# Performance work log

Measured on AMD Instinct MI355X. Metric: run time of the kernel, lower is better.

The kernel has to match this reference:

```python
import jax, jax.numpy as jnp
import numpy as np

E = 128        # EMBEDDING_DIM
H = 8          # HEAD_NUM
K = 16         # KEY_DIM
NODE = 200     # NODE_SIZE
CLIP = 10.0    # LOGIT_CLIPPING
B = 256
G = 200        # group size
S = 100        # solution tokens


def setup_inputs() -> dict:
    key = jax.random.key(0)
    ks = jax.random.split(key, 9)
    sc = 1.0 / np.sqrt(E)
    return {
        "graph": jax.random.normal(ks[0], (B, 1, E), jnp.float32),
        "capacity": jax.random.uniform(ks[1], (B, G), jnp.float32),
        "sols_mask_pomo": jnp.zeros((B, G, S), jnp.float32),
        "ninf_mask": jnp.zeros((B, G, NODE), jnp.float32),
        "encoded_nodes": jax.random.normal(ks[2], (B, NODE + S, E), jnp.float32),
        "Wq": jax.random.normal(ks[3], (1 + E, H * K), jnp.float32) * sc,
        "Wk": jax.random.normal(ks[4], (E, H * K), jnp.float32) * sc,
        "Wv": jax.random.normal(ks[5], (E, H * K), jnp.float32) * sc,
        "Wc": jax.random.normal(ks[6], (H * K, E), jnp.float32) * sc,
        "bc": jax.random.normal(ks[7], (E,), jnp.float32) * sc,
        "Wk_logit": jax.random.normal(ks[8], (E, E), jnp.float32) * sc,
    }


def _heads(x):
    # [B, C, H*K] -> [B, H, C, K]
    b, c, _ = x.shape
    return x.reshape(b, c, H, K).transpose(0, 2, 1, 3)


def _mha(q, k, v, group_ninf_mask):
    # q: [B,H,n,K], k/v: [B,H,m,K], mask: [B,n,m]
    score = jnp.einsum("bhnk,bhmk->bhnm", q, k) / np.sqrt(K)
    score = score + group_ninf_mask[:, None, :, :]
    w = jax.nn.softmax(score, axis=-1)
    out = jnp.einsum("bhnm,bhmk->bhnk", w, v)          # [B,H,n,K]
    b, _, n, _ = out.shape
    return out.transpose(0, 2, 1, 3).reshape(b, n, H * K)


def reference(graph, capacity, sols_mask_pomo, ninf_mask, encoded_nodes,
              Wq, Wk, Wv, Wc, bc, Wk_logit):
    nodes, sols = encoded_nodes[:, :NODE], encoded_nodes[:, NODE:]
    # reset(): NOTE original uses Wk/Wv for solution tokens too
    k = _heads(nodes @ Wk)
    v = _heads(nodes @ Wv)
    k_s = _heads(sols @ Wk)
    v_s = _heads(sols @ Wv)
    single_head_key = nodes @ Wk_logit                   # [B, NODE, E]

    b, g = capacity.shape
    inp = jnp.concatenate(
        [jnp.broadcast_to(graph, (b, g, E)), capacity[:, :, None]], axis=2)
    q = _heads(inp @ Wq)                                 # [B,H,G,K]

    out_n = _mha(q, k, v, ninf_mask)
    out_s = _mha(q, k_s, v_s, sols_mask_pomo)
    mh = (out_n + out_s) @ Wc + bc                       # [B,G,E]

    score = jnp.einsum("bge,bne->bgn", mh, single_head_key) / np.sqrt(E)
    score = CLIP * jnp.tanh(score) + ninf_mask
    return jax.nn.softmax(score, axis=2)
```

## Files before the change

kernel.cpp:

```cpp
#include <hip/hip_runtime.h>

#define B_    256
#define G_    200
#define S_    100
#define NODE_ 200
#define E_    128
#define H_    8
#define M_    300
#define MT_   19
#define NT_   13

typedef float    f32x4 __attribute__((ext_vector_type(4)));
typedef short    s16x4 __attribute__((ext_vector_type(4)));
typedef short    s16x8 __attribute__((ext_vector_type(8)));
typedef unsigned u32x4 __attribute__((ext_vector_type(4)));

#define MFMA16(A, B, C) __builtin_amdgcn_mfma_f32_16x16x32_bf16(A, B, C, 0, 0, 0)

#define LOG2E_  1.4426950408889634f
#define CQ_     0.36067376022224085f
#define C2T_    0.25503901628148863f
#define C10L_   14.426950408889634f

__device__ __forceinline__ unsigned bf16u(float x) {
    unsigned u = __builtin_bit_cast(unsigned, x);
    return (u + 0x7fffu + ((u >> 16) & 1u)) >> 16;
}
__device__ __forceinline__ float bfbits(unsigned hb16) {
    return __builtin_bit_cast(float, hb16 << 16);
}
__device__ __forceinline__ short bfhi(float x) { return (short)bf16u(x); }
__device__ __forceinline__ short bflo(float x, short hi) {
    float hf = __builtin_bit_cast(float, ((unsigned)(unsigned short)hi) << 16);
    return (short)bf16u(x - hf);
}
__device__ __forceinline__ unsigned cvtpk(float a, float b) {
    unsigned r;
    asm("v_cvt_pk_bf16_f32 %0, %1, %2" : "=v"(r) : "v"(a), "v"(b));
    return r;
}
__device__ __forceinline__ float exp2a(float x) {
    float r;
    asm("v_exp_f32 %0, %1" : "=v"(r) : "v"(x));
    return r;
}
__device__ __forceinline__ s16x8 cat8(s16x4 a, s16x4 b) {
    s16x8 r; r[0]=a[0]; r[1]=a[1]; r[2]=a[2]; r[3]=a[3];
             r[4]=b[0]; r[5]=b[1]; r[6]=b[2]; r[7]=b[3]; return r;
}
__device__ __forceinline__ void split_pack(f32x4 v, s16x8& B1, s16x8& B2) {
    unsigned h01 = cvtpk(v[0], v[1]);
    unsigned h23 = cvtpk(v[2], v[3]);
    float e0 = v[0] - __builtin_bit_cast(float, h01 << 16);
    float e1 = v[1] - __builtin_bit_cast(float, h01 & 0xffff0000u);
    float e2 = v[2] - __builtin_bit_cast(float, h23 << 16);
    float e3 = v[3] - __builtin_bit_cast(float, h23 & 0xffff0000u);
    unsigned l01 = cvtpk(e0, e1), l23 = cvtpk(e2, e3);
    u32x4 w1 = {h01, h23, l01, l23};
    u32x4 w2 = {l01, l23, h01, h23};
    B1 = __builtin_bit_cast(s16x8, w1);
    B2 = __builtin_bit_cast(s16x8, w2);
}
__device__ __forceinline__ void pack8(f32x4 a0, f32x4 a1, s16x8& Bh, s16x8& Bl) {
    unsigned ha = cvtpk(a0[0], a0[1]), hb = cvtpk(a0[2], a0[3]);
    unsigned hc = cvtpk(a1[0], a1[1]), hd = cvtpk(a1[2], a1[3]);
    float e0 = a0[0] - __builtin_bit_cast(float, ha << 16);
    float e1 = a0[1] - __builtin_bit_cast(float, ha & 0xffff0000u);
    float e2 = a0[2] - __builtin_bit_cast(float, hb << 16);
    float e3 = a0[3] - __builtin_bit_cast(float, hb & 0xffff0000u);
    float e4 = a1[0] - __builtin_bit_cast(float, hc << 16);
    float e5 = a1[1] - __builtin_bit_cast(float, hc & 0xffff0000u);
    float e6 = a1[2] - __builtin_bit_cast(float, hd << 16);
    float e7 = a1[3] - __builtin_bit_cast(float, hd & 0xffff0000u);
    unsigned la = cvtpk(e0, e1), lb = cvtpk(e2, e3);
    unsigned lc = cvtpk(e4, e5), ld = cvtpk(e6, e7);
    u32x4 wh = {ha, hb, hc, hd}, wl = {la, lb, lc, ld};
    Bh = __builtin_bit_cast(s16x8, wh);
    Bl = __builtin_bit_cast(s16x8, wl);
}

__global__ __launch_bounds__(64) void wfrag_kernel(
    const float* __restrict__ Wk, const float* __restrict__ Wv,
    const float* __restrict__ Wl, const float* __restrict__ Wc,
    short* __restrict__ wf8_hi, short* __restrict__ wf8_lo)
{
    const int p = blockIdx.x, ct = blockIdx.y;
    const int l = threadIdx.x, qq = l >> 4, li = l & 15;
    const float* W = (p == 0) ? Wk : ((p == 1) ? Wv : ((p == 2) ? Wl : Wc));
    for (int kc = 0; kc < 8; ++kc) {
        s16x4 hi, lo;
        #pragma unroll
        for (int j = 0; j < 4; ++j) {
            float v = W[(kc*16 + qq*4 + j)*E_ + ct*16 + li];
            short h = bfhi(v); hi[j] = h; lo[j] = bflo(v, h);
        }
        const int ix = (((p*8 + ct)*4 + (kc >> 1))*64 + l)*8 + (kc & 1)*4;
        *(s16x4*)(wf8_hi + ix) = hi;
        *(s16x4*)(wf8_lo + ix) = lo;
    }
}

__global__ __launch_bounds__(128) void qbase_kernel(
    const float* __restrict__ graph, const float* __restrict__ Wq,
    float* __restrict__ qbase)
{
    const int b = blockIdx.x, c = threadIdx.x;
    __shared__ float gs[E_];
    gs[c] = graph[b*E_ + c];
    __syncthreads();
    float acc = 0.f;
    #pragma unroll 8
    for (int e = 0; e < E_; ++e) acc += gs[e] * Wq[e*E_ + c];
    qbase[b*E_ + c] = acc;
}

__global__ __launch_bounds__(64, 4) void proj_kernel(
    const float* __restrict__ enc,
    const short* __restrict__ wf8_hi, const short* __restrict__ wf8_lo,
    short* __restrict__ kf_il, short* __restrict__ vf_il,
    short* __restrict__ sf8_hi, short* __restrict__ sf8_lo)
{
    int id = blockIdx.x;
    { const int xcd = id & 7, pos = id >> 3; id = xcd*608 + pos; }
    const int b = id / MT_, mt = id % MT_;
    const int l = threadIdx.x, qq = l >> 4, li = l & 15;
    const int m = mt*16 + li;

    s16x8 Ahi[4], Alo[4];
    #pragma unroll
    for (int u = 0; u < 4; ++u) {
        float va[8];
        if (m < M_) {
            const float* ep = enc + ((size_t)b*M_ + m)*E_ + u*32 + qq*4;
            float4 f0 = *(const float4*)ep;
            float4 f1 = *(const float4*)(ep + 16);
            va[0]=f0.x; va[1]=f0.y; va[2]=f0.z; va[3]=f0.w;
            va[4]=f1.x; va[5]=f1.y; va[6]=f1.z; va[7]=f1.w;
        } else {
            #pragma unroll
            for (int j = 0; j < 8; ++j) va[j] = 0.f;
        }
        #pragma unroll
        for (int j = 0; j < 8; ++j) {
            short h = bfhi(va[j]); Ahi[u][j] = h; Alo[u][j] = bflo(va[j], h);
        }
    }

    __shared__ unsigned tile[16*17];

    #pragma unroll
    for (int p = 0; p < 3; ++p) {
        if (p == 2 && mt >= NT_) break;
        #pragma unroll
        for (int ct = 0; ct < 8; ++ct) {
            f32x4 acc = {0.f, 0.f, 0.f, 0.f};
            #pragma unroll
            for (int u = 0; u < 4; ++u) {
                const int base = (((p*8 + ct)*4 + u)*64 + l)*8;
                s16x8 Bh = *(const s16x8*)(wf8_hi + base);
                s16x8 Bl = *(const s16x8*)(wf8_lo + base);
                acc = MFMA16(Ahi[u], Bh, acc);
                acc = MFMA16(Ahi[u], Bl, acc);
                acc = MFMA16(Alo[u], Bh, acc);
            }
            if (p == 1) {
                s16x4 oh, ol;
                #pragma unroll
                for (int r = 0; r < 4; ++r) { short h = bfhi(acc[r]); oh[r] = h; ol[r] = bflo(acc[r], h); }
                const size_t ix = (((size_t)(b*8 + ct))*MT_ + mt)*512 + (size_t)l*8;
                *(s16x8*)(vf_il + ix) = cat8(oh, ol);
            } else {
                #pragma unroll
                for (int r = 0; r < 4; ++r) {
                    short h = bfhi(acc[r]); short lo = bflo(acc[r], h);
                    tile[(qq*4 + r)*17 + li] = (((unsigned)(unsigned short)h) << 16) | (unsigned short)(unsigned)lo;
                }
                __syncthreads();
                s16x4 oh, ol;
                #pragma unroll
                for (int j = 0; j < 4; ++j) {
                    unsigned wv = tile[li*17 + qq*4 + j];
                    oh[j] = (short)(wv >> 16); ol[j] = (short)(wv & 0xffffu);
                }
                if (p == 0) {
                    const size_t ix = (((size_t)(b*8 + ct))*MT_ + mt)*512 + (size_t)l*8;
                    *(s16x8*)(kf_il + ix) = cat8(oh, ol);
                } else {
                    const size_t ix = (((size_t)(b*NT_ + mt))*4 + (ct >> 1))*512 + (size_t)l*8 + (ct & 1)*4;
                    *(s16x4*)(sf8_hi + ix) = oh;
                    *(s16x4*)(sf8_lo + ix) = ol;
                }
                __syncthreads();
            }
        }
    }
}

__global__ __launch_bounds__(256, 3) void attn1_kernel(
    const float* __restrict__ capacity, const float* __restrict__ sols_mask,
    const float* __restrict__ ninf_mask, const float* __restrict__ Wq,
    const float* __restrict__ qbase,
    const short* __restrict__ kf_il, const short* __restrict__ vf_il,
    float* __restrict__ outws)
{
    int id = blockIdx.x;
    { const int xcd = id & 7, pos = id >> 3; id = xcd*416 + pos; }
    const int b = id / NT_, gt = id % NT_;
    const int t = threadIdx.x;
    const int w = t >> 6, l = t & 63, qq = l >> 4, li = l & 15;
    const int g0 = gt*16;

    __shared__ unsigned mlds[MT_][64][2];

    {
        const size_t bg = (size_t)b*G_;
        for (int f = t; f < 1600; f += 256) {
            const int g = f/100, p = f - g*100;
            int gg = g0 + g; gg = (gg < G_) ? gg : G_-1;
            float2 v = *(const float2*)(ninf_mask + (bg + gg)*NODE_ + p*2);
            const int mm = p*2;
            mlds[mm>>4][((mm>>2)&3)*16 + g][(mm>>1)&1] = cvtpk(v.x*LOG2E_, v.y*LOG2E_);
        }
        for (int f = t; f < 800; f += 256) {
            const int g = f/50, p = f - g*50;
            int gg = g0 + g; gg = (gg < G_) ? gg : G_-1;
            float2 v = *(const float2*)(sols_mask + (bg + gg)*S_ + p*2);
            const int mm = 200 + p*2;
            mlds[mm>>4][((mm>>2)&3)*16 + g][(mm>>1)&1] = cvtpk(v.x*LOG2E_, v.y*LOG2E_);
        }
        if (t < 32) {
            mlds[18][48 + (t>>1)][t&1] = 0xFF80FF80u;
        }
    }
    __syncthreads();

    int ggl = g0 + li; ggl = (ggl < G_) ? ggl : G_-1;
    const float cap = capacity[b*G_ + ggl];
    const bool isN12 = (qq < 2);

    #pragma unroll 1
    for (int hi2 = 0; hi2 < 2; ++hi2) {
        const int h = w*2 + hi2;
        s16x8 qB1, qB2;
        {
            float4 qb4 = *(const float4*)(qbase + b*E_ + h*16 + qq*4);
            float4 wl4 = *(const float4*)(Wq + E_*E_ + h*16 + qq*4);
            f32x4 qv = {qb4.x + cap*wl4.x, qb4.y + cap*wl4.y,
                        qb4.z + cap*wl4.z, qb4.w + cap*wl4.w};
            split_pack(qv, qB1, qB2);
        }
        f32x4 sc[MT_];
        const size_t kb = ((size_t)(b*8 + h)*MT_)*512 + (size_t)l*8;
        #pragma unroll
        for (int mt = 0; mt < MT_; ++mt) {
            s16x8 kf8 = *(const s16x8*)(kf_il + kb + (size_t)mt*512);
            f32x4 a = {0.f, 0.f, 0.f, 0.f};
            a = MFMA16(kf8, qB1, a);
            a = MFMA16(kf8, qB2, a);
            sc[mt] = a;
        }
        f32x4 sA = {0.f,0.f,0.f,0.f}, sB = {0.f,0.f,0.f,0.f}, sC = {0.f,0.f,0.f,0.f};
        #pragma unroll
        for (int mt = 0; mt < MT_; ++mt) {
            const uint2 mp = *(const uint2*)&mlds[mt][l][0];
            f32x4 e;
            e[0] = exp2a(fmaf(sc[mt][0], CQ_, bfbits(mp.x & 0xffffu)));
            e[1] = exp2a(fmaf(sc[mt][1], CQ_, bfbits(mp.x >> 16)));
            e[2] = exp2a(fmaf(sc[mt][2], CQ_, bfbits(mp.y & 0xffffu)));
            e[3] = exp2a(fmaf(sc[mt][3], CQ_, bfbits(mp.y >> 16)));
            sc[mt] = e;
            if (mt < 12)       { if (mt & 1) sB += e; else sA += e; }
            else if (mt > 12)  sC += e;
        }
        float s12 = (sc[12][0] + sc[12][1]) + (sc[12][2] + sc[12][3]);
        f32x4 sAB = sA + sB;
        float sN = (sAB[0] + sAB[1]) + (sAB[2] + sAB[3]) + (isN12 ? s12 : 0.f);
        float sS = (sC[0] + sC[1]) + (sC[2] + sC[3]) + (isN12 ? 0.f : s12);
        sN += __shfl_xor(sN, 16); sN += __shfl_xor(sN, 32);
        sS += __shfl_xor(sS, 16); sS += __shfl_xor(sS, 32);
        const float rN = 1.f / sN, rS = 1.f / sS;
        { const float r12 = isN12 ? rN : rS; sc[12] *= r12; }

        f32x4 oN0 = {0.f,0.f,0.f,0.f}, oN1 = {0.f,0.f,0.f,0.f};
        f32x4 oS0 = {0.f,0.f,0.f,0.f}, oS1 = {0.f,0.f,0.f,0.f};
        f32x4 o12 = {0.f,0.f,0.f,0.f};
        #pragma unroll
        for (int mt = 0; mt < MT_; ++mt) {
            s16x8 pB1, pB2;
            split_pack(sc[mt], pB1, pB2);
            s16x8 vf8 = *(const s16x8*)(vf_il + kb + (size_t)mt*512);
            f32x4& acc = (mt < 12) ? ((mt & 1) ? oN1 : oN0)
                       : (mt == 12 ? o12 : ((mt & 1) ? oS1 : oS0));
            acc = MFMA16(vf8, pB1, acc);
            acc = MFMA16(vf8, pB2, acc);
        }
        f32x4 on = oN0 + oN1, os = oS0 + oS1, osum;
        #pragma unroll
        for (int r = 0; r < 4; ++r)
            osum[r] = fmaf(on[r], rN, fmaf(os[r], rS, o12[r]));

        *(f32x4*)(outws + (((size_t)(b*NT_ + gt))*8 + h)*256 + (size_t)l*4) = osum;
    }
}

__global__ __launch_bounds__(64, 4) void attn2_kernel(
    const float* __restrict__ ninf_mask,
    const short* __restrict__ sf8_hi, const short* __restrict__ sf8_lo,
    const short* __restrict__ wf8_hi, const short* __restrict__ wf8_lo,
    const float* __restrict__ bc_,
    const float* __restrict__ outws,
    float* __restrict__ out)
{
    int id = blockIdx.x;
    { const int xcd = id & 7, pos = id >> 3; id = xcd*416 + pos; }
    const int b = id / NT_, gt = id % NT_;
    const int l = threadIdx.x, qq = l >> 4, li = l & 15;
    const int g0 = gt*16;

    __shared__ float pool[16*308];

    {
        const size_t bg = (size_t)b*G_;
        for (int f = l; f < 800; f += 64) {
            const int g = f/50, p = f - g*50;
            int gg = g0 + g; gg = (gg < G_) ? gg : G_-1;
            *(float4*)&pool[g*308 + p*4] = *(const float4*)(ninf_mask + (bg + gg)*NODE_ + p*4);
        }
    }
    __syncthreads();

    s16x8 BhO[4], BlO[4];
    #pragma unroll
    for (int u = 0; u < 4; ++u) {
        f32x4 a0 = *(const f32x4*)(outws + (((size_t)(b*NT_ + gt))*8 + 2*u)*256 + (size_t)l*4);
        f32x4 a1 = *(const f32x4*)(outws + (((size_t)(b*NT_ + gt))*8 + 2*u + 1)*256 + (size_t)l*4);
        pack8(a0, a1, BhO[u], BlO[u]);
    }
    s16x8 Bh2[4], Bl2[4];
    #pragma unroll
    for (int u = 0; u < 4; ++u) {
        f32x4 t01[2];
        #pragma unroll
        for (int half = 0; half < 2; ++half) {
            const int jt = 2*u + half;
            f32x4 acc = {0.f, 0.f, 0.f, 0.f};
            #pragma unroll
            for (int uu = 0; uu < 4; ++uu) {
                const int base = (((3*8 + jt)*4 + uu)*64 + l)*8;
                s16x8 Ah = *(const s16x8*)(wf8_hi + base);
                s16x8 Al = *(const s16x8*)(wf8_lo + base);
                acc = MFMA16(Ah, BhO[uu], acc);
                acc = MFMA16(Ah, BlO[uu], acc);
                acc = MFMA16(Al, BhO[uu], acc);
            }
            float4 b4 = *(const float4*)(bc_ + jt*16 + qq*4);
            acc[0] += b4.x; acc[1] += b4.y; acc[2] += b4.z; acc[3] += b4.w;
            t01[half] = acc;
        }
        pack8(t01[0], t01[1], Bh2[u], Bl2[u]);
    }
    f32x4 z[NT_];
    #pragma unroll
    for (int nt = 0; nt < NT_; ++nt) {
        f32x4 acc = {0.f, 0.f, 0.f, 0.f};
        #pragma unroll
        for (int u = 0; u < 4; ++u) {
            const size_t base = (((size_t)(b*NT_ + nt))*4 + u)*512 + (size_t)l*8;
            s16x8 Ah = *(const s16x8*)(sf8_hi + base);
            s16x8 Al = *(const s16x8*)(sf8_lo + base);
            acc = MFMA16(Ah, Bh2[u], acc);
            acc = MFMA16(Ah, Bl2[u], acc);
            acc = MFMA16(Al, Bh2[u], acc);
        }
        z[nt] = acc;
    }
    float sm = 0.f;
    #pragma unroll
    for (int nt = 0; nt < NT_; ++nt) {
        f32x4 mk = *(const f32x4*)&pool[li*308 + nt*16 + qq*4];
        f32x4 e;
        #pragma unroll
        for (int r = 0; r < 4; ++r) {
            if (nt < 12 || (qq*4 + r) < 8) {
                float ex = exp2a(z[nt][r] * C2T_);
                float th = 1.f - 2.f / (ex + 1.f);
                e[r] = exp2a(fmaf(th, C10L_, mk[r]*LOG2E_));
            } else e[r] = 0.f;
        }
        z[nt] = e;
        sm += (e[0] + e[1]) + (e[2] + e[3]);
    }
    sm += __shfl_xor(sm, 16); sm += __shfl_xor(sm, 32);
    const float rs = 1.f / sm;

    float* ob = out + (size_t)b*G_*NODE_;
    __syncthreads();
    #pragma unroll
    for (int ch = 0; ch < 4; ++ch) {
        const int ntn = (ch < 3) ? 4 : 1;
        for (int k = 0; k < ntn; ++k) {
            const int nt = ch*4 + k;
            #pragma unroll
            for (int r = 0; r < 4; ++r)
                pool[li*69 + k*16 + qq*4 + r] = z[nt][r] * rs;
        }
        __syncthreads();
        const int n = ch*64 + l;
        const bool nok = (ch < 3) || (l < 8);
        #pragma unroll
        for (int gi = 0; gi < 16; ++gi) {
            const int g = g0 + gi;
            if (nok && g < G_) ob[(size_t)g*NODE_ + n] = pool[gi*69 + l];
        }
        __syncthreads();
    }
}

extern "C" void kernel_launch(void* const* d_in, const int* in_sizes, int n_in,
                              void* d_out, int out_size, void* d_ws, size_t ws_size,
                              hipStream_t stream) {
    (void)in_sizes; (void)n_in; (void)out_size; (void)ws_size;
    const float* graph = (const float*)d_in[0];
    const float* capacity = (const float*)d_in[1];
    const float* sols_mask = (const float*)d_in[2];
    const float* ninf_mask = (const float*)d_in[3];
    const float* enc = (const float*)d_in[4];
    const float* Wq  = (const float*)d_in[5];
    const float* Wk  = (const float*)d_in[6];
    const float* Wv  = (const float*)d_in[7];
    const float* Wc  = (const float*)d_in[8];
    const float* bc  = (const float*)d_in[9];
    const float* Wkl = (const float*)d_in[10];
    float* out = (float*)d_out;

    char* wsb = (char*)d_ws;
    short* kf_il  = (short*)(wsb);
    short* sf8_hi = (short*)(wsb + 39845888);
    short* sf8_lo = (short*)(wsb + 53477376);
    short* wf8_hi = (short*)(wsb + 67108864);
    short* wf8_lo = (short*)(wsb + 67239936);
    float* qb     = (float*)(wsb + 67371008);
    float* outws  = (float*)(wsb + 67502080);
    short* vf_il  = (short*)d_out;

    wfrag_kernel<<<dim3(4, 8), 64, 0, stream>>>(Wk, Wv, Wkl, Wc, wf8_hi, wf8_lo);
    qbase_kernel<<<B_, 128, 0, stream>>>(graph, Wq, qb);
    proj_kernel<<<MT_*B_, 64, 0, stream>>>(enc, wf8_hi, wf8_lo, kf_il, vf_il, sf8_hi, sf8_lo);
    attn1_kernel<<<NT_*B_, 256, 0, stream>>>(capacity, sols_mask, ninf_mask, Wq, qb,
                                             kf_il, vf_il, outws);
    attn2_kernel<<<NT_*B_, 64, 0, stream>>>(ninf_mask, sf8_hi, sf8_lo, wf8_hi, wf8_lo,
                                            bc, outws, out);
}
```

Before: 209.1 us.

## Stream attention tiles to cut register use, raise occupancy, pack masks as bf16

```diff
diff --git a/kernel.cpp b/kernel.cpp
--- a/kernel.cpp
+++ b/kernel.cpp
@@ -22,6 +22,22 @@
 #define C2T_    0.25503901628148863f
 #define C10L_   14.426950408889634f
 
+#if defined(__has_builtin)
+#  if __has_builtin(__builtin_amdgcn_exp2f)
+#    define EXP2_BUILTIN 1
+#  endif
+#endif
+
+__device__ __forceinline__ float exp2a(float x) {
+#ifdef EXP2_BUILTIN
+    return __builtin_amdgcn_exp2f(x);
+#else
+    float r;
+    asm("v_exp_f32 %0, %1" : "=v"(r) : "v"(x));
+    return r;
+#endif
+}
+
 __device__ __forceinline__ unsigned bf16u(float x) {
     unsigned u = __builtin_bit_cast(unsigned, x);
     return (u + 0x7fffu + ((u >> 16) & 1u)) >> 16;
@@ -37,11 +53,6 @@
 __device__ __forceinline__ unsigned cvtpk(float a, float b) {
     unsigned r;
     asm("v_cvt_pk_bf16_f32 %0, %1, %2" : "=v"(r) : "v"(a), "v"(b));
-    return r;
-}
-__device__ __forceinline__ float exp2a(float x) {
-    float r;
-    asm("v_exp_f32 %0, %1" : "=v"(r) : "v"(x));
     return r;
 }
 __device__ __forceinline__ s16x8 cat8(s16x4 a, s16x4 b) {
@@ -196,7 +207,7 @@
     }
 }
 
-__global__ __launch_bounds__(256, 3) void attn1_kernel(
+__global__ __launch_bounds__(256, 6) void attn1_kernel(
     const float* __restrict__ capacity, const float* __restrict__ sols_mask,
     const float* __restrict__ ninf_mask, const float* __restrict__ Wq,
     const float* __restrict__ qbase,
@@ -249,55 +260,80 @@
                         qb4.z + cap*wl4.z, qb4.w + cap*wl4.w};
             split_pack(qv, qB1, qB2);
         }
-        f32x4 sc[MT_];
-        const size_t kb = ((size_t)(b*8 + h)*MT_)*512 + (size_t)l*8;
-        #pragma unroll
-        for (int mt = 0; mt < MT_; ++mt) {
-            s16x8 kf8 = *(const s16x8*)(kf_il + kb + (size_t)mt*512);
-            f32x4 a = {0.f, 0.f, 0.f, 0.f};
-            a = MFMA16(kf8, qB1, a);
-            a = MFMA16(kf8, qB2, a);
-            sc[mt] = a;
-        }
-        f32x4 sA = {0.f,0.f,0.f,0.f}, sB = {0.f,0.f,0.f,0.f}, sC = {0.f,0.f,0.f,0.f};
-        #pragma unroll
-        for (int mt = 0; mt < MT_; ++mt) {
-            const uint2 mp = *(const uint2*)&mlds[mt][l][0];
-            f32x4 e;
-            e[0] = exp2a(fmaf(sc[mt][0], CQ_, bfbits(mp.x & 0xffffu)));
-            e[1] = exp2a(fmaf(sc[mt][1], CQ_, bfbits(mp.x >> 16)));
-            e[2] = exp2a(fmaf(sc[mt][2], CQ_, bfbits(mp.y & 0xffffu)));
-            e[3] = exp2a(fmaf(sc[mt][3], CQ_, bfbits(mp.y >> 16)));
-            sc[mt] = e;
-            if (mt < 12)       { if (mt & 1) sB += e; else sA += e; }
-            else if (mt > 12)  sC += e;
-        }
-        float s12 = (sc[12][0] + sc[12][1]) + (sc[12][2] + sc[12][3]);
-        f32x4 sAB = sA + sB;
-        float sN = (sAB[0] + sAB[1]) + (sAB[2] + sAB[3]) + (isN12 ? s12 : 0.f);
-        float sS = (sC[0] + sC[1]) + (sC[2] + sC[3]) + (isN12 ? 0.f : s12);
+        const short* kfb = kf_il + ((size_t)(b*8 + h)*MT_)*512 + (size_t)l*8;
+        const short* vfb = vf_il + ((size_t)(b*8 + h)*MT_)*512 + (size_t)l*8;
+
+        f32x4 oN0 = {0.f,0.f,0.f,0.f}, oN1 = {0.f,0.f,0.f,0.f};
+        f32x4 oS0 = {0.f,0.f,0.f,0.f}, oS1 = {0.f,0.f,0.f,0.f};
+        f32x4 vsN = {0.f,0.f,0.f,0.f}, vsS = {0.f,0.f,0.f,0.f};
+        float s12 = 0.f;
+        const f32x4 zz = {0.f,0.f,0.f,0.f};
+
+        #pragma unroll
+        for (int gp = 0; gp < 10; ++gp) {
+            const int mA = 2*gp, mB = 2*gp + 1;
+            s16x8 kfA = *(const s16x8*)(kfb + (size_t)mA*512);
+            s16x8 vfA = *(const s16x8*)(vfb + (size_t)mA*512);
+            s16x8 kfB = {0,0,0,0,0,0,0,0}, vfB = {0,0,0,0,0,0,0,0};
+            if (gp < 9) {
+                kfB = *(const s16x8*)(kfb + (size_t)mB*512);
+                vfB = *(const s16x8*)(vfb + (size_t)mB*512);
+            }
+            f32x4 sa = MFMA16(kfA, qB1, zz); sa = MFMA16(kfA, qB2, sa);
+            f32x4 sb = zz;
+            if (gp < 9) { sb = MFMA16(kfB, qB1, zz); sb = MFMA16(kfB, qB2, sb); }
+
+            const uint2 mpa = *(const uint2*)&mlds[mA][l][0];
+            f32x4 ea;
+            ea[0] = exp2a(fmaf(sa[0], CQ_, bfbits(mpa.x & 0xffffu)));
+            ea[1] = exp2a(fmaf(sa[1], CQ_, bfbits(mpa.x >> 16)));
+            ea[2] = exp2a(fmaf(sa[2], CQ_, bfbits(mpa.y & 0xffffu)));
+            ea[3] = exp2a(fmaf(sa[3], CQ_, bfbits(mpa.y >> 16)));
+            if (mA == 12) {
+                s12 = (ea[0] + ea[1]) + (ea[2] + ea[3]);
+                f32x4 eN, eS;
+                #pragma unroll
+                for (int r = 0; r < 4; ++r) {
+                    eN[r] = isN12 ? ea[r] : 0.f;
+                    eS[r] = isN12 ? 0.f : ea[r];
+                }
+                s16x8 pN1, pN2, pS1, pS2;
+                split_pack(eN, pN1, pN2);
+                split_pack(eS, pS1, pS2);
+                oN0 = MFMA16(vfA, pN1, oN0); oN0 = MFMA16(vfA, pN2, oN0);
+                oS0 = MFMA16(vfA, pS1, oS0); oS0 = MFMA16(vfA, pS2, oS0);
+            } else {
+                if (mA < 12) vsN += ea; else vsS += ea;
+                s16x8 pA1, pA2;
+                split_pack(ea, pA1, pA2);
+                f32x4& acc = (mA < 12) ? oN0 : oS0;
+                acc = MFMA16(vfA, pA1, acc);
+                acc = MFMA16(vfA, pA2, acc);
+            }
+            if (gp < 9) {
+                const uint2 mpb = *(const uint2*)&mlds[mB][l][0];
+                f32x4 eb;
+                eb[0] = exp2a(fmaf(sb[0], CQ_, bfbits(mpb.x & 0xffffu)));
+                eb[1] = exp2a(fmaf(sb[1], CQ_, bfbits(mpb.x >> 16)));
+                eb[2] = exp2a(fmaf(sb[2], CQ_, bfbits(mpb.y & 0xffffu)));
+                eb[3] = exp2a(fmaf(sb[3], CQ_, bfbits(mpb.y >> 16)));
+                if (mB < 12) vsN += eb; else vsS += eb;
+                s16x8 pB1, pB2;
+                split_pack(eb, pB1, pB2);
+                f32x4& acc2 = (mB < 12) ? oN1 : oS1;
+                acc2 = MFMA16(vfB, pB1, acc2);
+                acc2 = MFMA16(vfB, pB2, acc2);
+            }
+        }
+        float sN = (vsN[0] + vsN[1]) + (vsN[2] + vsN[3]) + (isN12 ? s12 : 0.f);
+        float sS = (vsS[0] + vsS[1]) + (vsS[2] + vsS[3]) + (isN12 ? 0.f : s12);
         sN += __shfl_xor(sN, 16); sN += __shfl_xor(sN, 32);
         sS += __shfl_xor(sS, 16); sS += __shfl_xor(sS, 32);
         const float rN = 1.f / sN, rS = 1.f / sS;
-        { const float r12 = isN12 ? rN : rS; sc[12] *= r12; }
-
-        f32x4 oN0 = {0.f,0.f,0.f,0.f}, oN1 = {0.f,0.f,0.f,0.f};
-        f32x4 oS0 = {0.f,0.f,0.f,0.f}, oS1 = {0.f,0.f,0.f,0.f};
-        f32x4 o12 = {0.f,0.f,0.f,0.f};
-        #pragma unroll
-        for (int mt = 0; mt < MT_; ++mt) {
-            s16x8 pB1, pB2;
-            split_pack(sc[mt], pB1, pB2);
-            s16x8 vf8 = *(const s16x8*)(vf_il + kb + (size_t)mt*512);
-            f32x4& acc = (mt < 12) ? ((mt & 1) ? oN1 : oN0)
-                       : (mt == 12 ? o12 : ((mt & 1) ? oS1 : oS0));
-            acc = MFMA16(vf8, pB1, acc);
-            acc = MFMA16(vf8, pB2, acc);
-        }
         f32x4 on = oN0 + oN1, os = oS0 + oS1, osum;
         #pragma unroll
         for (int r = 0; r < 4; ++r)
-            osum[r] = fmaf(on[r], rN, fmaf(os[r], rS, o12[r]));
+            osum[r] = fmaf(on[r], rN, os[r]*rS);
 
         *(f32x4*)(outws + (((size_t)(b*NT_ + gt))*8 + h)*256 + (size_t)l*4) = osum;
     }
@@ -317,14 +353,15 @@
     const int l = threadIdx.x, qq = l >> 4, li = l & 15;
     const int g0 = gt*16;
 
-    __shared__ float pool[16*308];
+    __shared__ unsigned mpool[16*104];
 
     {
         const size_t bg = (size_t)b*G_;
-        for (int f = l; f < 800; f += 64) {
-            const int g = f/50, p = f - g*50;
+        for (int f = l; f < 1600; f += 64) {
+            const int g = f/100, p = f - g*100;
             int gg = g0 + g; gg = (gg < G_) ? gg : G_-1;
-            *(float4*)&pool[g*308 + p*4] = *(const float4*)(ninf_mask + (bg + gg)*NODE_ + p*4);
+            float2 v = *(const float2*)(ninf_mask + (bg + gg)*NODE_ + p*2);
+            mpool[g*104 + p] = cvtpk(v.x*LOG2E_, v.y*LOG2E_);
         }
     }
     __syncthreads();
@@ -377,14 +414,16 @@
     float sm = 0.f;
     #pragma unroll
     for (int nt = 0; nt < NT_; ++nt) {
-        f32x4 mk = *(const f32x4*)&pool[li*308 + nt*16 + qq*4];
+        const uint2 mp = *(const uint2*)&mpool[li*104 + ((nt*8 + qq*2 < 100) ? nt*8 + qq*2 : 0)];
         f32x4 e;
         #pragma unroll
         for (int r = 0; r < 4; ++r) {
             if (nt < 12 || (qq*4 + r) < 8) {
                 float ex = exp2a(z[nt][r] * C2T_);
                 float th = 1.f - 2.f / (ex + 1.f);
-                e[r] = exp2a(fmaf(th, C10L_, mk[r]*LOG2E_));
+                const unsigned mb = (r == 0) ? (mp.x & 0xffffu) : (r == 1) ? (mp.x >> 16)
+                                  : (r == 2) ? (mp.y & 0xffffu) : (mp.y >> 16);
+                e[r] = exp2a(fmaf(th, C10L_, bfbits(mb)));
             } else e[r] = 0.f;
         }
         z[nt] = e;
@@ -393,6 +432,7 @@
     sm += __shfl_xor(sm, 16); sm += __shfl_xor(sm, 32);
     const float rs = 1.f / sm;
 
+    float* tbuf = (float*)mpool;
     float* ob = out + (size_t)b*G_*NODE_;
     __syncthreads();
     #pragma unroll
@@ -402,7 +442,7 @@
             const int nt = ch*4 + k;
             #pragma unroll
             for (int r = 0; r < 4; ++r)
-                pool[li*69 + k*16 + qq*4 + r] = z[nt][r] * rs;
+                tbuf[li*69 + k*16 + qq*4 + r] = z[nt][r] * rs;
         }
         __syncthreads();
         const int n = ch*64 + l;
@@ -410,7 +450,7 @@
         #pragma unroll
         for (int gi = 0; gi < 16; ++gi) {
             const int g = g0 + gi;
-            if (nok && g < G_) ob[(size_t)g*NODE_ + n] = pool[gi*69 + l];
+            if (nok && g < G_) ob[(size_t)g*NODE_ + n] = tbuf[gi*69 + l];
         }
         __syncthreads();
     }
```

Measured after the change: 173.9 us. 1.2x faster.
